# Optimization experiments

Hardware: AMD Instinct MI355X
Metric: run time of the kernel (lower is better)

The kernel has to match this reference:

```python
import jax, jax.numpy as jnp
import numpy as np

QWEN_H = 2048
SNN_H = 512


def setup_inputs() -> dict:
    key = jax.random.key(0)
    k0, k1, k2, k3, k4 = jax.random.split(key, 5)
    hidden_states = jax.random.normal(k0, (4, 2048, QWEN_H), dtype=jnp.float32)
    # nn.Linear weights stored as [out, in]
    w_down = jax.random.normal(k1, (SNN_H, QWEN_H), dtype=jnp.float32) / np.sqrt(QWEN_H)
    w_up = jax.random.normal(k2, (QWEN_H, SNN_H), dtype=jnp.float32) / np.sqrt(SNN_H)
    w1 = jax.random.normal(k3, (SNN_H, SNN_H), dtype=jnp.float32) / np.sqrt(SNN_H)
    w2 = jax.random.normal(k4, (SNN_H, SNN_H), dtype=jnp.float32) / np.sqrt(SNN_H)
    residual_scale = jnp.float32(0.1)
    return {"hidden_states": hidden_states, "w_down": w_down, "w_up": w_up,
            "w1": w1, "w2": w2, "residual_scale": residual_scale}


def reference(hidden_states, w_down, w_up, w1, w2, residual_scale):
    # Faithful math of SNNMiddleLayer.forward. The spike pulse encode ->
    # SpikeFP32Linear (fp32 accumulation) -> pulse decode path is a lossless
    # FP32 spike encoding of an ordinary bias-free linear layer, so the
    # per-timestep loop computes exactly out_t = w2 @ (w1 @ proj_down(x_t)),
    # which we express as fused batched GEMMs over all timesteps.
    residual = hidden_states
    x = jnp.einsum('bsq,hq->bsh', hidden_states, w_down)   # proj_down
    h = jnp.einsum('bsh,oh->bso', x, w1)                   # snn_linear1
    o = jnp.einsum('bso,po->bsp', h, w2)                   # snn_linear2
    out = jnp.einsum('bsp,qp->bsq', o, w_up)               # proj_up
    return residual + residual_scale * out
```

## Files before the change

kernel.cpp:

```cpp
#include <hip/hip_runtime.h>
#include <hip/hip_bf16.h>
#include <stdint.h>

using bf16 = __hip_bfloat16;
typedef __attribute__((ext_vector_type(8))) short bf16x8;
typedef __attribute__((ext_vector_type(4))) float f32x4;

__device__ __forceinline__ void async_load16(const void* g, void* l) {
    __builtin_amdgcn_global_load_lds(
        (__attribute__((address_space(1))) const void*)g,
        (__attribute__((address_space(3))) void*)l,
        16, 0, 0);
}

__device__ __forceinline__ void cvt_block_2048(const float* __restrict__ src,
                                               bf16* __restrict__ dst, int relblk) {
    int i = (relblk * 256 + (int)threadIdx.x) * 8;
    float4 f0 = *(const float4*)(src + i);
    float4 f1 = *(const float4*)(src + i + 4);
    union { bf16 h[8]; uint4 u; } o;
    o.h[0] = __float2bfloat16(f0.x); o.h[1] = __float2bfloat16(f0.y);
    o.h[2] = __float2bfloat16(f0.z); o.h[3] = __float2bfloat16(f0.w);
    o.h[4] = __float2bfloat16(f1.x); o.h[5] = __float2bfloat16(f1.y);
    o.h[6] = __float2bfloat16(f1.z); o.h[7] = __float2bfloat16(f1.w);
    *(uint4*)(dst + i) = o.u;
}

__global__ __launch_bounds__(256) void prep_w(
    const float* __restrict__ w1, bf16* __restrict__ w1b,
    const float* __restrict__ wup, bf16* __restrict__ wub,
    const float* __restrict__ wd, bf16* __restrict__ wdt,
    const float* __restrict__ w2, bf16* __restrict__ w2t) {
    __shared__ bf16 sh[32][33];
    int b = blockIdx.x;
    if (b < 128)       { cvt_block_2048(w1, w1b, b); return; }
    if (b < 640)       { cvt_block_2048(wup, wub, b - 128); return; }
    const float* src; bf16* dst; int R, C, tile, ntx;
    if (b < 1664) { src = wd; dst = wdt; R = 512; C = 2048; tile = b - 640; ntx = 64; }
    else          { src = w2; dst = w2t; R = 512; C = 512;  tile = b - 1664; ntx = 16; }
    const int bx = (tile % ntx) * 32, by = (tile / ntx) * 32;
    const int lx = threadIdx.x & 31;
    const int ly4 = ((int)threadIdx.x >> 5) * 4;
#pragma unroll
    for (int r = 0; r < 4; ++r)
        sh[ly4 + r][lx] = __float2bfloat16(src[(size_t)(by + ly4 + r) * C + bx + lx]);
    __syncthreads();
#pragma unroll
    for (int r = 0; r < 4; ++r)
        dst[(size_t)(bx + ly4 + r) * R + by + lx] = sh[lx][ly4 + r];
}

template<int BN, int EPI, int NP>
__device__ __forceinline__ void gemm_core(
    const bf16* __restrict__ A, const bf16* __restrict__ B,
    bf16* __restrict__ Cb, float* __restrict__ Cf,
    const float* __restrict__ Res, const float* __restrict__ sp,
    int N, int K, int bxi, int byi, bf16* As, bf16* Bs)
{
    constexpr int BM = 128;
    constexpr int NJ = BN / 32;
    static_assert(BN == 64 || BN == 128, "BN");

    const int tid  = threadIdx.x;
    const int wave = tid >> 6;
    const int lane = tid & 63;
    const int wm = wave >> 1, wn = wave & 1;
    const size_t bm = (size_t)bxi * BM;
    const size_t bn = (size_t)byi * BN;

    f32x4 acc[4][NJ];
#pragma unroll
    for (int i = 0; i < 4; ++i)
#pragma unroll
        for (int j = 0; j < NJ; ++j)
            acc[i][j] = (f32x4){0.f, 0.f, 0.f, 0.f};

    const int srow  = lane >> 3;
    const int scol8 = (lane & 7) ^ srow;

    float4 res_pre[EPI ? 8 : 1];
    if (EPI) {
        const int r16 = lane >> 3;
        const int cbb = (lane & 7) * 4;
#pragma unroll
        for (int i = 0; i < 2; ++i)
#pragma unroll
            for (int rh = 0; rh < 2; ++rh)
#pragma unroll
                for (int ch = 0; ch < 2; ++ch) {
                    size_t row = bm + wm * 64 + i * 16 + rh * 8 + r16;
                    size_t col = bn + wn * 64 + cbb + ch * 32;
                    res_pre[i * 4 + rh * 2 + ch] = *(const float4*)&Res[row * (size_t)N + col];
                }
    }

    for (int k0 = 0; k0 < K; k0 += 64 * NP) {
        constexpr int TOT = (BM + BN) / 8;
#pragma unroll
        for (int p = 0; p < NP; ++p)
#pragma unroll
            for (int c = 0; c < TOT / 4; ++c) {
                const int cc = wave + c * 4;
                if (cc < BM / 8) {
                    const int rb = cc * 8;
                    async_load16(A + (bm + rb + srow) * (size_t)K + k0 + p * 64 + scol8 * 8,
                                 &As[p * BM * 64 + rb * 64]);
                } else {
                    const int rb = (cc - BM / 8) * 8;
                    async_load16(B + (bn + rb + srow) * (size_t)K + k0 + p * 64 + scol8 * 8,
                                 &Bs[p * BN * 64 + rb * 64]);
                }
            }
        __syncthreads();

#pragma unroll
        for (int kk = 0; kk < 2 * NP; ++kk) {
            const bf16* Ap = As + (kk >> 1) * BM * 64;
            const bf16* Bp = Bs + (kk >> 1) * BN * 64;
            const int c8 = (kk & 1) * 4 + (lane >> 4);
            bf16x8 af[4], bfr[NJ];
#pragma unroll
            for (int i = 0; i < 4; ++i) {
                const int r = wm * 64 + i * 16 + (lane & 15);
                af[i] = *(const bf16x8*)&Ap[(size_t)(r * 8 + (c8 ^ (r & 7))) * 8];
            }
#pragma unroll
            for (int j = 0; j < NJ; ++j) {
                const int r = wn * (BN / 2) + j * 16 + (lane & 15);
                bfr[j] = *(const bf16x8*)&Bp[(size_t)(r * 8 + (c8 ^ (r & 7))) * 8];
            }
#pragma unroll
            for (int i = 0; i < 4; ++i)
#pragma unroll
                for (int j = 0; j < NJ; ++j)
                    acc[i][j] = __builtin_amdgcn_mfma_f32_16x16x32_bf16(af[i], bfr[j], acc[i][j], 0, 0, 0);
        }
        __syncthreads();
    }

    const int col_l = lane & 15;
    const int row_l = (lane >> 4) * 4;
    if (EPI == 0) {
#pragma unroll
        for (int i = 0; i < 4; ++i)
#pragma unroll
            for (int j = 0; j < NJ; ++j)
#pragma unroll
                for (int r = 0; r < 4; ++r) {
                    size_t row = bm + wm * 64 + i * 16 + row_l + r;
                    size_t col = bn + wn * (BN / 2) + j * 16 + col_l;
                    Cb[row * (size_t)N + col] = __float2bfloat16(acc[i][j][r]);
                }
    } else {
        const float s = *sp;
        float* lds_f = (float*)As + wave * (16 * 68);
#pragma unroll
        for (int i = 0; i < 4; ++i) {
#pragma unroll
            for (int j = 0; j < NJ; ++j)
#pragma unroll
                for (int r = 0; r < 4; ++r)
                    lds_f[(row_l + r) * 68 + j * 16 + col_l] = acc[i][j][r];
            __syncthreads();
#pragma unroll
            for (int rh = 0; rh < 2; ++rh)
#pragma unroll
                for (int ch = 0; ch < 2; ++ch) {
                    const int r16 = rh * 8 + (lane >> 3);
                    const int cb  = (lane & 7) * 4 + ch * 32;
                    float4 v = *(float4*)&lds_f[r16 * 68 + cb];
                    size_t row = bm + wm * 64 + i * 16 + r16;
                    size_t col = bn + wn * 64 + cb;
                    size_t idx = row * (size_t)N + col;
                    float4 rv = (i < 2) ? res_pre[i * 4 + rh * 2 + ch]
                                        : *(const float4*)&Res[idx];
                    float4 o;
                    o.x = rv.x + s * v.x; o.y = rv.y + s * v.y;
                    o.z = rv.z + s * v.z; o.w = rv.w + s * v.w;
                    *(float4*)&Cf[idx] = o;
                }
            __syncthreads();
        }
    }
}

template<int BN, int EPI, int NP>
__global__ __launch_bounds__(256) void gemm_bf16(
    const bf16* __restrict__ A, const bf16* __restrict__ B,
    bf16* __restrict__ Cb, float* __restrict__ Cf,
    const float* __restrict__ Res, const float* __restrict__ sp, int N, int K) {
    __shared__ __align__(16) bf16 smem[(128 + BN) * 64 * NP];
    gemm_core<BN, EPI, NP>(A, B, Cb, Cf, Res, sp, N, K, blockIdx.y, blockIdx.x,
                           smem, smem + 128 * 64 * NP);
}

__global__ __launch_bounds__(256) void ru_cvt(
    const bf16* __restrict__ A0, const bf16* __restrict__ B0, bf16* __restrict__ C0,
    const bf16* __restrict__ A1, const bf16* __restrict__ B1, bf16* __restrict__ C1,
    const float* __restrict__ hs, bf16* __restrict__ hsb) {
    __shared__ __align__(16) bf16 smem[(128 + 64) * 64];
    int b = blockIdx.x;
    if (b < 128)
        gemm_core<64, 0, 1>(A0, B0, C0, nullptr, nullptr, nullptr, 2048, 512,
                            b / 32, b % 32, smem, smem + 128 * 64);
    else if (b < 256) {
        int bb = b - 128;
        gemm_core<64, 0, 1>(A1, B1, C1, nullptr, nullptr, nullptr, 512, 512,
                            bb / 8, bb % 8, smem, smem + 128 * 64);
    } else
        cvt_block_2048(hs, hsb, b - 256);
}

extern "C" void kernel_launch(void* const* d_in, const int* in_sizes, int n_in,
                              void* d_out, int out_size, void* d_ws, size_t ws_size,
                              hipStream_t stream) {
    const float* hs     = (const float*)d_in[0];
    const float* w_down = (const float*)d_in[1];
    const float* w_up   = (const float*)d_in[2];
    const float* w1     = (const float*)d_in[3];
    const float* w2     = (const float*)d_in[4];
    const float* rs     = (const float*)d_in[5];

    char* ws = (char*)d_ws;
    bf16* hs_b  = (bf16*)(ws + 0);
    bf16* x_b   = (bf16*)(ws + 33554432);
    bf16* w1_b  = (bf16*)(ws + 41943040);
    bf16* wu_b  = (bf16*)(ws + 42467328);
    bf16* wdt_b = (bf16*)(ws + 44564480);
    bf16* w2t_b = (bf16*)(ws + 46661632);
    bf16* Rm    = (bf16*)(ws + 47185920);
    bf16* Um    = (bf16*)(ws + 49283072);

    prep_w<<<dim3(1920), dim3(256), 0, stream>>>(w1, w1_b, w_up, wu_b, w_down, wdt_b, w2, w2t_b);
    ru_cvt<<<dim3(256 + 8192), dim3(256), 0, stream>>>(w1_b, wdt_b, Rm, wu_b, w2t_b, Um, hs, hs_b);
    gemm_bf16<64, 0, 2><<<dim3(8, 64), dim3(256), 0, stream>>>(hs_b, Rm, x_b, nullptr,
                                                               nullptr, nullptr, 512, 2048);
    gemm_bf16<128, 1, 1><<<dim3(16, 64), dim3(256), 0, stream>>>(x_b, Um, nullptr, (float*)d_out,
                                                                 hs, rs, 2048, 512);
}
```

Before: 211.3 us.

## Double-buffer LDS tiles to overlap async global loads with MFMA compute

Replaces the load-then-compute K loop with a two-buffer ping-pong: the next K tile is issued via async global-to-LDS loads while MFMAs run on the current one. The first GEMM switches from a 128-wide K step to 64, and the output GEMM uses a 32-wide K step with a new swizzle to keep LDS usage bounded. This is meant to hide global memory latency behind compute, at the cost of more loop iterations and barriers and a larger LDS footprint in ru_cvt. Loads go straight to LDS, so correctness relies on the barrier at the end of each iteration waiting for them to complete.

```diff
diff --git a/kernel.cpp b/kernel.cpp
--- a/kernel.cpp
+++ b/kernel.cpp
@@ -50,16 +50,61 @@
         dst[(size_t)(bx + ly4 + r) * R + by + lx] = sh[lx][ly4 + r];
 }
 
-template<int BN, int EPI, int NP>
+template<int BN, int BK>
+__device__ __forceinline__ void stage_tiles(
+    const bf16* __restrict__ A, const bf16* __restrict__ B,
+    size_t bm, size_t bn, int K, int k0,
+    bf16* __restrict__ As, bf16* __restrict__ Bs, int wave, int lane)
+{
+    if constexpr (BK == 64) {
+        const int srow = lane >> 3;
+        const int scol = (lane & 7) ^ srow;
+        constexpr int NCH = (128 + BN) / 8;
+#pragma unroll
+        for (int c = 0; c < NCH / 4; ++c) {
+            const int cc = wave + c * 4;
+            if (cc < 16) {
+                const int rb = cc * 8;
+                async_load16(A + (bm + rb + srow) * (size_t)K + k0 + scol * 8,
+                             &As[rb * 64]);
+            } else {
+                const int rb = (cc - 16) * 8;
+                async_load16(B + (bn + rb + srow) * (size_t)K + k0 + scol * 8,
+                             &Bs[rb * 64]);
+            }
+        }
+    } else {
+        const int sr = lane >> 2;
+        const int sc = (lane & 3) ^ ((sr >> 1) & 3);
+        constexpr int NCH = (128 + BN) / 16;
+#pragma unroll
+        for (int c = 0; c < NCH / 4; ++c) {
+            const int cc = wave + c * 4;
+            if (cc < 8) {
+                const int rb = cc * 16;
+                async_load16(A + (bm + rb + sr) * (size_t)K + k0 + sc * 8,
+                             &As[rb * 32]);
+            } else {
+                const int rb = (cc - 8) * 16;
+                async_load16(B + (bn + rb + sr) * (size_t)K + k0 + sc * 8,
+                             &Bs[rb * 32]);
+            }
+        }
+    }
+}
+
+template<int BN, int EPI, int BK>
 __device__ __forceinline__ void gemm_core(
     const bf16* __restrict__ A, const bf16* __restrict__ B,
     bf16* __restrict__ Cb, float* __restrict__ Cf,
     const float* __restrict__ Res, const float* __restrict__ sp,
-    int N, int K, int bxi, int byi, bf16* As, bf16* Bs)
+    int N, int K, int bxi, int byi, bf16* smem)
 {
     constexpr int BM = 128;
     constexpr int NJ = BN / 32;
+    constexpr int BUF = (BM + BN) * BK;
     static_assert(BN == 64 || BN == 128, "BN");
+    static_assert(BK == 32 || BK == 64, "BK");
 
     const int tid  = threadIdx.x;
     const int wave = tid >> 6;
@@ -75,9 +120,6 @@
         for (int j = 0; j < NJ; ++j)
             acc[i][j] = (f32x4){0.f, 0.f, 0.f, 0.f};
 
-    const int srow  = lane >> 3;
-    const int scol8 = (lane & 7) ^ srow;
-
     float4 res_pre[EPI ? 8 : 1];
     if (EPI) {
         const int r16 = lane >> 3;
@@ -94,40 +136,51 @@
                 }
     }
 
-    for (int k0 = 0; k0 < K; k0 += 64 * NP) {
-        constexpr int TOT = (BM + BN) / 8;
-#pragma unroll
-        for (int p = 0; p < NP; ++p)
-#pragma unroll
-            for (int c = 0; c < TOT / 4; ++c) {
-                const int cc = wave + c * 4;
-                if (cc < BM / 8) {
-                    const int rb = cc * 8;
-                    async_load16(A + (bm + rb + srow) * (size_t)K + k0 + p * 64 + scol8 * 8,
-                                 &As[p * BM * 64 + rb * 64]);
-                } else {
-                    const int rb = (cc - BM / 8) * 8;
-                    async_load16(B + (bn + rb + srow) * (size_t)K + k0 + p * 64 + scol8 * 8,
-                                 &Bs[p * BN * 64 + rb * 64]);
-                }
-            }
-        __syncthreads();
-
-#pragma unroll
-        for (int kk = 0; kk < 2 * NP; ++kk) {
-            const bf16* Ap = As + (kk >> 1) * BM * 64;
-            const bf16* Bp = Bs + (kk >> 1) * BN * 64;
-            const int c8 = (kk & 1) * 4 + (lane >> 4);
+    stage_tiles<BN, BK>(A, B, bm, bn, K, 0, smem, smem + BM * BK, wave, lane);
+    __syncthreads();
+
+    int cur = 0;
+    for (int k0 = 0; k0 < K; k0 += BK) {
+        if (k0 + BK < K) {
+            bf16* nb = smem + (cur ^ 1) * BUF;
+            stage_tiles<BN, BK>(A, B, bm, bn, K, k0 + BK, nb, nb + BM * BK, wave, lane);
+        }
+        const bf16* Ap = smem + cur * BUF;
+        const bf16* Bp = Ap + BM * BK;
+
+        if constexpr (BK == 64) {
+#pragma unroll
+            for (int kk = 0; kk < 2; ++kk) {
+                const int c8 = kk * 4 + (lane >> 4);
+                bf16x8 af[4], bfr[NJ];
+#pragma unroll
+                for (int i = 0; i < 4; ++i) {
+                    const int r = wm * 64 + i * 16 + (lane & 15);
+                    af[i] = *(const bf16x8*)&Ap[(size_t)(r * 8 + (c8 ^ (r & 7))) * 8];
+                }
+#pragma unroll
+                for (int j = 0; j < NJ; ++j) {
+                    const int r = wn * (BN / 2) + j * 16 + (lane & 15);
+                    bfr[j] = *(const bf16x8*)&Bp[(size_t)(r * 8 + (c8 ^ (r & 7))) * 8];
+                }
+#pragma unroll
+                for (int i = 0; i < 4; ++i)
+#pragma unroll
+                    for (int j = 0; j < NJ; ++j)
+                        acc[i][j] = __builtin_amdgcn_mfma_f32_16x16x32_bf16(af[i], bfr[j], acc[i][j], 0, 0, 0);
+            }
+        } else {
+            const int c4 = lane >> 4;
             bf16x8 af[4], bfr[NJ];
 #pragma unroll
             for (int i = 0; i < 4; ++i) {
                 const int r = wm * 64 + i * 16 + (lane & 15);
-                af[i] = *(const bf16x8*)&Ap[(size_t)(r * 8 + (c8 ^ (r & 7))) * 8];
+                af[i] = *(const bf16x8*)&Ap[(size_t)(r * 4 + (c4 ^ ((r >> 1) & 3))) * 8];
             }
 #pragma unroll
             for (int j = 0; j < NJ; ++j) {
                 const int r = wn * (BN / 2) + j * 16 + (lane & 15);
-                bfr[j] = *(const bf16x8*)&Bp[(size_t)(r * 8 + (c8 ^ (r & 7))) * 8];
+                bfr[j] = *(const bf16x8*)&Bp[(size_t)(r * 4 + (c4 ^ ((r >> 1) & 3))) * 8];
             }
 #pragma unroll
             for (int i = 0; i < 4; ++i)
@@ -136,6 +189,7 @@
                     acc[i][j] = __builtin_amdgcn_mfma_f32_16x16x32_bf16(af[i], bfr[j], acc[i][j], 0, 0, 0);
         }
         __syncthreads();
+        cur ^= 1;
     }
 
     const int col_l = lane & 15;
@@ -153,7 +207,7 @@
                 }
     } else {
         const float s = *sp;
-        float* lds_f = (float*)As + wave * (16 * 68);
+        float* lds_f = (float*)smem + wave * (16 * 68);
 #pragma unroll
         for (int i = 0; i < 4; ++i) {
 #pragma unroll
@@ -184,29 +238,28 @@
     }
 }
 
-template<int BN, int EPI, int NP>
+template<int BN, int EPI, int BK>
 __global__ __launch_bounds__(256) void gemm_bf16(
     const bf16* __restrict__ A, const bf16* __restrict__ B,
     bf16* __restrict__ Cb, float* __restrict__ Cf,
     const float* __restrict__ Res, const float* __restrict__ sp, int N, int K) {
-    __shared__ __align__(16) bf16 smem[(128 + BN) * 64 * NP];
-    gemm_core<BN, EPI, NP>(A, B, Cb, Cf, Res, sp, N, K, blockIdx.y, blockIdx.x,
-                           smem, smem + 128 * 64 * NP);
+    __shared__ __align__(16) bf16 smem[(128 + BN) * BK * 2];
+    gemm_core<BN, EPI, BK>(A, B, Cb, Cf, Res, sp, N, K, blockIdx.y, blockIdx.x, smem);
 }
 
 __global__ __launch_bounds__(256) void ru_cvt(
     const bf16* __restrict__ A0, const bf16* __restrict__ B0, bf16* __restrict__ C0,
     const bf16* __restrict__ A1, const bf16* __restrict__ B1, bf16* __restrict__ C1,
     const float* __restrict__ hs, bf16* __restrict__ hsb) {
-    __shared__ __align__(16) bf16 smem[(128 + 64) * 64];
+    __shared__ __align__(16) bf16 smem[(128 + 64) * 64 * 2];
     int b = blockIdx.x;
     if (b < 128)
-        gemm_core<64, 0, 1>(A0, B0, C0, nullptr, nullptr, nullptr, 2048, 512,
-                            b / 32, b % 32, smem, smem + 128 * 64);
+        gemm_core<64, 0, 64>(A0, B0, C0, nullptr, nullptr, nullptr, 2048, 512,
+                             b / 32, b % 32, smem);
     else if (b < 256) {
         int bb = b - 128;
-        gemm_core<64, 0, 1>(A1, B1, C1, nullptr, nullptr, nullptr, 512, 512,
-                            bb / 8, bb % 8, smem, smem + 128 * 64);
+        gemm_core<64, 0, 64>(A1, B1, C1, nullptr, nullptr, nullptr, 512, 512,
+                             bb / 8, bb % 8, smem);
     } else
         cvt_block_2048(hs, hsb, b - 256);
 }
@@ -233,8 +286,8 @@
 
     prep_w<<<dim3(1920), dim3(256), 0, stream>>>(w1, w1_b, w_up, wu_b, w_down, wdt_b, w2, w2t_b);
     ru_cvt<<<dim3(256 + 8192), dim3(256), 0, stream>>>(w1_b, wdt_b, Rm, wu_b, w2t_b, Um, hs, hs_b);
-    gemm_bf16<64, 0, 2><<<dim3(8, 64), dim3(256), 0, stream>>>(hs_b, Rm, x_b, nullptr,
-                                                               nullptr, nullptr, 512, 2048);
-    gemm_bf16<128, 1, 1><<<dim3(16, 64), dim3(256), 0, stream>>>(x_b, Um, nullptr, (float*)d_out,
-                                                                 hs, rs, 2048, 512);
-}
+    gemm_bf16<64, 0, 64><<<dim3(8, 64), dim3(256), 0, stream>>>(hs_b, Rm, x_b, nullptr,
+                                                                nullptr, nullptr, 512, 2048);
+    gemm_bf16<128, 1, 32><<<dim3(16, 64), dim3(256), 0, stream>>>(x_b, Um, nullptr, (float*)d_out,
+                                                                  hs, rs, 2048, 512);
+}
```

After: 211.3 us. About the same (+0.0%).
